# Optimization experiments

Measured on AMD Instinct MI355X. Metric: run time of the kernel, lower is better.

The kernel has to match this reference:

```python
import jax, jax.numpy as jnp
import numpy as np

B, T, D, N = 32, 2048, 512, 512


def setup_inputs() -> dict:
    key = jax.random.key(0)
    ks = jax.random.split(key, 16)
    s_in = 1.0 / np.sqrt(D)
    s_h = 1.0 / np.sqrt(N)
    inp = {
        "x": jax.random.normal(ks[0], (B, T, D), dtype=jnp.float32),
        "W_i": jax.random.normal(ks[1], (D, N), dtype=jnp.float32) * s_in,
        "U_i": jax.random.normal(ks[2], (N, N), dtype=jnp.float32) * s_h,
        "W_f": jax.random.normal(ks[3], (D, N), dtype=jnp.float32) * s_in,
        "U_f": jax.random.normal(ks[4], (N, N), dtype=jnp.float32) * s_h,
        "W_g": jax.random.normal(ks[5], (D, N), dtype=jnp.float32) * s_in,
        "U_g": jax.random.normal(ks[6], (N, N), dtype=jnp.float32) * s_h,
        "W_c": jax.random.normal(ks[7], (D, N), dtype=jnp.float32) * s_in,
        "U_c": jax.random.normal(ks[8], (N, N), dtype=jnp.float32) * s_h,
        "W_o": jax.random.normal(ks[9], (N, N), dtype=jnp.float32) * s_h,
        "b_i": jnp.zeros((N,), dtype=jnp.float32),
        "b_f": jnp.zeros((N,), dtype=jnp.float32),
        "b_g": jnp.zeros((N,), dtype=jnp.float32),
        "b_c": jnp.zeros((N,), dtype=jnp.float32),
        "b_o": jnp.zeros((N,), dtype=jnp.float32),
    }
    return inp


def _lstm_forward(x, W_i, U_i, W_f, U_f, W_g, U_g, W_c, U_c, W_o,
                  b_i, b_f, b_g, b_c, b_o):
    # Precompute input-to-gate projections for all timesteps (same math,
    # hoisted out of the recurrence): [T, B, N] each
    xt = jnp.swapaxes(x, 0, 1)  # [T, B, N? no, D] -> [T, B, D]
    xi = jnp.einsum('tbd,dn->tbn', xt, W_i) + b_i
    xf = jnp.einsum('tbd,dn->tbn', xt, W_f) + b_f
    xg = jnp.einsum('tbd,dn->tbn', xt, W_g) + b_g
    xc = jnp.einsum('tbd,dn->tbn', xt, W_c) + b_c

    h0 = jnp.zeros((x.shape[0], U_i.shape[0]), dtype=x.dtype)
    c0 = jnp.zeros_like(h0)

    def step(carry, gates_t):
        h, c = carry
        xi_t, xf_t, xg_t, xc_t = gates_t
        i = jax.nn.sigmoid(xi_t + h @ U_i)
        f = jax.nn.sigmoid(xf_t + h @ U_f)
        g = jax.nn.sigmoid(xg_t + h @ U_g)  # original applies nonlin_i to g
        c_tilda = jnp.tanh(xc_t + h @ U_c)
        c_new = f * c + i * c_tilda
        h_new = g * jnp.tanh(c_new)
        return (h_new, c_new), h_new

    _, hs = jax.lax.scan(step, (h0, c0), (xi, xf, xg, xc))  # hs: [T, B, N]
    # output_fn: relu(h @ W_o + b_o), applied per timestep
    out = jax.nn.relu(jnp.einsum('tbn,nm->tbm', hs, W_o) + b_o)
    return jnp.swapaxes(out, 0, 1)  # [B, T, N]


def reference(x, W_i, U_i, W_f, U_f, W_g, U_g, W_c, U_c, W_o,
              b_i, b_f, b_g, b_c, b_o):
    return _lstm_forward(x, W_i, U_i, W_f, U_f, W_g, U_g, W_c, U_c, W_o,
                         b_i, b_f, b_g, b_c, b_o)
```

## Files before the change

### kernel.cpp

```cpp
#include <hip/hip_runtime.h>
#include <stdint.h>

#define B_ 32
#define T_ 2048
#define D_ 512
#define N_ 512
#define NG 2048

typedef _Float16 f16;
typedef _Float16 half2v __attribute__((ext_vector_type(2)));
typedef _Float16 half8  __attribute__((ext_vector_type(8)));
typedef float    float4v __attribute__((ext_vector_type(4)));
typedef unsigned long long u64;

union U32H2 { unsigned u; half2v h; };
union U4H8  { uint4 u; half8 h; };
union H16U  { f16 h; unsigned short s; };

__global__ void prep_cast(const float* __restrict__ x, f16* __restrict__ x16) {
    long i = ((long)blockIdx.x * 256 + threadIdx.x) * 4;
    float4 v = *(const float4*)(x + i);
    union { f16 h[4]; uint2 u; } pk;
    pk.h[0] = (f16)v.x; pk.h[1] = (f16)v.y; pk.h[2] = (f16)v.z; pk.h[3] = (f16)v.w;
    *(uint2*)(x16 + i) = pk.u;
}

__global__ void prep_w(const float* __restrict__ Wi, const float* __restrict__ Ui,
                       const float* __restrict__ Wf, const float* __restrict__ Uf,
                       const float* __restrict__ Wg, const float* __restrict__ Ug,
                       const float* __restrict__ Wc, const float* __restrict__ Uc,
                       const float* __restrict__ Wo,
                       const float* __restrict__ bi, const float* __restrict__ bff,
                       const float* __restrict__ bg, const float* __restrict__ bc,
                       f16* __restrict__ wt, f16* __restrict__ ut,
                       f16* __restrict__ wot, float* __restrict__ bias)
{
    const int y = blockIdx.y;
    const int e = blockIdx.x * 256 + threadIdx.x;
    if (y < 4) {
        const float* src = (y == 0) ? Wi : (y == 1) ? Wf : (y == 2) ? Wg : Wc;
        int col = e >> 9, d = e & 511;
        wt[(long)y * 512 * 512 + e] = (f16)src[(long)d * 512 + col];
    } else if (y < 8) {
        const float* src = (y == 4) ? Ui : (y == 5) ? Uf : (y == 6) ? Ug : Uc;
        int col = e >> 9, d = e & 511;
        ut[(long)(y - 4) * 512 * 512 + e] = (f16)src[(long)d * 512 + col];
    } else if (y == 8) {
        int col = e >> 9, d = e & 511;
        wot[e] = (f16)Wo[(long)d * 512 + col];
    } else {
        if (e < 2048) {
            const float* bsrc = (e < 512) ? bi : (e < 1024) ? bff : (e < 1536) ? bg : bc;
            bias[e] = bsrc[e & 511];
        }
    }
}

__launch_bounds__(256)
__global__ void gemm_xw(const f16* __restrict__ A, const f16* __restrict__ Bt,
                        const float* __restrict__ bias, f16* __restrict__ C)
{
    __shared__ f16 sA[128 * 32];
    __shared__ f16 sB[128 * 32];
    const int tid = threadIdx.x;
    const int m0 = blockIdx.y * 128;
    const int n0 = blockIdx.x * 128;
    const int wave = tid >> 6, lane = tid & 63;
    const int wm = wave >> 1, wn = wave & 1;
    const int lrow = lane & 15, quad = lane >> 4;

    float4v acc[4][4];
#pragma unroll
    for (int i = 0; i < 4; i++)
#pragma unroll
        for (int j = 0; j < 4; j++) acc[i][j] = (float4v){0.f, 0.f, 0.f, 0.f};

    const int srow = tid >> 2;
    const int sk8 = (tid & 3) * 8;

    for (int k0 = 0; k0 < 512; k0 += 32) {
#pragma unroll
        for (int rr = 0; rr < 128; rr += 64) {
            const int row = rr + srow;
            *(uint4*)&sA[row * 32 + sk8] = *(const uint4*)&A[(long)(m0 + row) * 512 + k0 + sk8];
            *(uint4*)&sB[row * 32 + sk8] = *(const uint4*)&Bt[(long)(n0 + row) * 512 + k0 + sk8];
        }
        __syncthreads();
        half8 af[4], bf[4];
#pragma unroll
        for (int mi = 0; mi < 4; mi++)
            af[mi] = *(half8*)&sA[(wm * 64 + mi * 16 + lrow) * 32 + quad * 8];
#pragma unroll
        for (int ni = 0; ni < 4; ni++)
            bf[ni] = *(half8*)&sB[(wn * 64 + ni * 16 + lrow) * 32 + quad * 8];
#pragma unroll
        for (int mi = 0; mi < 4; mi++)
#pragma unroll
            for (int ni = 0; ni < 4; ni++)
                acc[mi][ni] = __builtin_amdgcn_mfma_f32_16x16x32_f16(af[mi], bf[ni], acc[mi][ni], 0, 0, 0);
        __syncthreads();
    }
#pragma unroll
    for (int mi = 0; mi < 4; mi++)
#pragma unroll
        for (int ni = 0; ni < 4; ni++)
#pragma unroll
            for (int r = 0; r < 4; r++) {
                int m = m0 + wm * 64 + mi * 16 + quad * 4 + r;
                int n = n0 + wn * 64 + ni * 16 + lrow;
                C[(long)m * NG + n] = (f16)(acc[mi][ni][r] + bias[n]);
            }
}

__launch_bounds__(256)
__global__ void gemm_hw(const f16* __restrict__ A, const f16* __restrict__ Bt,
                        const float* __restrict__ bias, float* __restrict__ out)
{
    __shared__ f16 sA[128 * 32];
    __shared__ f16 sB[128 * 32];
    const int tid = threadIdx.x;
    const int m0 = blockIdx.y * 128;
    const int n0 = blockIdx.x * 128;
    const int wave = tid >> 6, lane = tid & 63;
    const int wm = wave >> 1, wn = wave & 1;
    const int lrow = lane & 15, quad = lane >> 4;

    float4v acc[4][4];
#pragma unroll
    for (int i = 0; i < 4; i++)
#pragma unroll
        for (int j = 0; j < 4; j++) acc[i][j] = (float4v){0.f, 0.f, 0.f, 0.f};

    const int srow = tid >> 2;
    const int sk8 = (tid & 3) * 8;

    for (int k0 = 0; k0 < 512; k0 += 32) {
#pragma unroll
        for (int rr = 0; rr < 128; rr += 64) {
            const int row = rr + srow;
            *(uint4*)&sA[row * 32 + sk8] = *(const uint4*)&A[(long)(m0 + row) * 512 + k0 + sk8];
            *(uint4*)&sB[row * 32 + sk8] = *(const uint4*)&Bt[(long)(n0 + row) * 512 + k0 + sk8];
        }
        __syncthreads();
        half8 af[4], bf[4];
#pragma unroll
        for (int mi = 0; mi < 4; mi++)
            af[mi] = *(half8*)&sA[(wm * 64 + mi * 16 + lrow) * 32 + quad * 8];
#pragma unroll
        for (int ni = 0; ni < 4; ni++)
            bf[ni] = *(half8*)&sB[(wn * 64 + ni * 16 + lrow) * 32 + quad * 8];
#pragma unroll
        for (int mi = 0; mi < 4; mi++)
#pragma unroll
            for (int ni = 0; ni < 4; ni++)
                acc[mi][ni] = __builtin_amdgcn_mfma_f32_16x16x32_f16(af[mi], bf[ni], acc[mi][ni], 0, 0, 0);
        __syncthreads();
    }
#pragma unroll
    for (int mi = 0; mi < 4; mi++)
#pragma unroll
        for (int ni = 0; ni < 4; ni++)
#pragma unroll
            for (int r = 0; r < 4; r++) {
                int m = m0 + wm * 64 + mi * 16 + quad * 4 + r;
                int n = n0 + wn * 64 + ni * 16 + lrow;
                float v = acc[mi][ni][r] + bias[n];
                v = fmaxf(v, 0.f);
                int t = m >> 5, b = m & 31;
                out[(long)b * (T_ * (long)N_) + (long)t * N_ + n] = v;
            }
}

__launch_bounds__(256, 1)
__global__ void lstm_rec(const f16* __restrict__ Ut,
                         const f16* __restrict__ xpre,
                         u64* __restrict__ hg64,
                         unsigned* __restrict__ hs32,
                         int unused)
{
    const int tid = threadIdx.x;
    const int bb = blockIdx.x & 31;
    const int s  = blockIdx.x >> 5;
    const int w    = tid >> 6;
    const int lane = tid & 63;
    const int quad = lane >> 4;
    const int lcol = lane & 15;

    __shared__ __align__(16) unsigned hbuf32[256];

    const int ncol = s * 64 + w * 16 + lcol;
    half8 bf[4][16];
#pragma unroll
    for (int g = 0; g < 4; g++) {
        const f16* bp = Ut + ((long)(g * 512 + ncol)) * 512 + quad * 8;
#pragma unroll
        for (int ks = 0; ks < 16; ks++)
            bf[g][ks] = *(const half8*)(bp + ks * 32);
    }

    hbuf32[tid] = 0u;
    float cst = 0.f;

    const f16* xb = xpre + (long)bb * T_ * NG + quad * 512 + ncol;
    f16 xcA = xb[0];
    f16 xcB = xb[NG];
    __syncthreads();

    const int pslot = s * 32 + w * 8 + (lane & 7);

#pragma unroll 1
    for (int t2 = 0; t2 < T_; t2 += 2) {
#pragma unroll
        for (int half = 0; half < 2; half++) {
            const int t = t2 + half;
            const f16 xuse = half ? xcB : xcA;

            if (t > 0) {
                const u64* slot = hg64 + (size_t)(t & 1) * 8192 + bb * 256 + tid;
                const unsigned tag = (unsigned)t;
                u64 v;
                while ((unsigned)((v = __hip_atomic_load(slot, __ATOMIC_RELAXED,
                                                         __HIP_MEMORY_SCOPE_AGENT)) >> 32) != tag) {}
                __builtin_amdgcn_sched_barrier(0);
                {
                    const long ti = (t + 2 < T_) ? (t + 2) : (T_ - 1);
                    const f16 xn = xb[ti * NG];
                    if (half) xcB = xn; else xcA = xn;
                }
                hbuf32[tid] = (unsigned)v;
            } else {
                const f16 xn = xb[2L * NG];
                xcA = xn;
            }

            asm volatile("s_waitcnt lgkmcnt(0)" ::: "memory");
            __builtin_amdgcn_s_barrier();
            __builtin_amdgcn_sched_barrier(0);

            float4v a0 = {0.f, 0.f, 0.f, 0.f}, a1 = {0.f, 0.f, 0.f, 0.f};
            float4v a2 = {0.f, 0.f, 0.f, 0.f}, a3 = {0.f, 0.f, 0.f, 0.f};
#pragma unroll
            for (int ks = 0; ks < 16; ks++) {
                U4H8 av;
                av.u = *(const uint4*)&hbuf32[ks * 16 + quad * 4];
                a0 = __builtin_amdgcn_mfma_f32_16x16x32_f16(av.h, bf[0][ks], a0, 0, 0, 0);
                a1 = __builtin_amdgcn_mfma_f32_16x16x32_f16(av.h, bf[1][ks], a1, 0, 0, 0);
                a2 = __builtin_amdgcn_mfma_f32_16x16x32_f16(av.h, bf[2][ks], a2, 0, 0, 0);
                a3 = __builtin_amdgcn_mfma_f32_16x16x32_f16(av.h, bf[3][ks], a3, 0, 0, 0);
            }

            float p01 = (quad == 0) ? a0[0] : a1[0];
            float p23 = (quad == 2) ? a2[0] : a3[0];
            float pre = ((quad < 2) ? p01 : p23) + (float)xuse;
            float m   = (quad == 3) ? 2.f : -1.f;
            float e   = __expf(m * pre);
            float r   = __builtin_amdgcn_rcpf(1.f + e);
            float act = (quad == 3) ? 1.f - 2.f * r : r;
            float b1 = __shfl_xor(act, 16);
            float b2 = __shfl_xor(act, 32);
            float b3 = __shfl_xor(b1, 32);
            float gi = (quad == 0) ? act : (quad == 1) ? b1 : (quad == 2) ? b2 : b3;
            float gf = (quad == 1) ? act : (quad == 0) ? b1 : (quad == 3) ? b2 : b3;
            float gg = (quad == 2) ? act : (quad == 3) ? b1 : (quad == 0) ? b2 : b3;
            float ct = (quad == 3) ? act : (quad == 2) ? b1 : (quad == 1) ? b2 : b3;

            cst = gf * cst + gi * ct;
            float e2 = __expf(2.f * cst);
            float th = 1.f - 2.f * __builtin_amdgcn_rcpf(1.f + e2);
            float h  = gg * th;

            H16U cv; cv.h = (f16)h;
            unsigned hx = (unsigned)cv.s;
            unsigned lo = __shfl(hx, 2 * (lane & 7));
            unsigned hi = __shfl(hx, 2 * (lane & 7) + 1);
            if (lane < 8) {
                unsigned pk = lo | (hi << 16);
                u64 pv = ((u64)(unsigned)(t + 1) << 32) | (u64)pk;
                __hip_atomic_store(hg64 + (size_t)((t + 1) & 1) * 8192 + bb * 256 + pslot,
                                   pv, __ATOMIC_RELAXED, __HIP_MEMORY_SCOPE_AGENT);
                hs32[((long)t * B_ + bb) * 256 + pslot] = pk;
            }

            __builtin_amdgcn_sched_barrier(0);
            __builtin_amdgcn_s_barrier();
        }
    }
}

extern "C" void kernel_launch(void* const* d_in, const int* in_sizes, int n_in,
                              void* d_out, int out_size, void* d_ws, size_t ws_size,
                              hipStream_t stream)
{
    const float* x  = (const float*)d_in[0];
    const float* Wi = (const float*)d_in[1];
    const float* Ui = (const float*)d_in[2];
    const float* Wf = (const float*)d_in[3];
    const float* Uf = (const float*)d_in[4];
    const float* Wg = (const float*)d_in[5];
    const float* Ug = (const float*)d_in[6];
    const float* Wc = (const float*)d_in[7];
    const float* Uc = (const float*)d_in[8];
    const float* Wo = (const float*)d_in[9];
    const float* bi = (const float*)d_in[10];
    const float* bf = (const float*)d_in[11];
    const float* bg = (const float*)d_in[12];
    const float* bc = (const float*)d_in[13];
    const float* bo = (const float*)d_in[14];

    char* ws = (char*)d_ws;
    f16*      x16   = (f16*)(ws + 0L);
    f16*      xpre  = (f16*)(ws + 67108864L);
    f16*      hs    = (f16*)(ws + 335544320L);
    f16*      wt    = (f16*)(ws + 402653184L);
    f16*      ut    = (f16*)(ws + 404750336L);
    f16*      wot   = (f16*)(ws + 406847488L);
    float*    bias  = (float*)(ws + 407371776L);
    u64*      hg64  = (u64*)(ws + 407379968L);

    prep_cast<<<dim3(32768), dim3(256), 0, stream>>>(x, x16);
    prep_w<<<dim3(1024, 10), dim3(256), 0, stream>>>(Wi, Ui, Wf, Uf, Wg, Ug, Wc, Uc, Wo,
                                                     bi, bf, bg, bc, wt, ut, wot, bias);
    gemm_xw<<<dim3(16, 512), dim3(256), 0, stream>>>(x16, wt, bias, xpre);
    lstm_rec<<<dim3(256), dim3(256), 0, stream>>>(ut, xpre, hg64, (unsigned*)hs, 0);
    gemm_hw<<<dim3(4, 512), dim3(256), 0, stream>>>(hs, wot, bo, (float*)d_out);
}
```

Baseline: 4.040 ms.

## Batch 16 sequences per recurrent block so MFMA rows carry real batches

The recurrent kernel is reorganized so each active block handles 16 batch elements and a 64-column slice across all four gates. This fills the 16 MFMA rows with real batch rows instead of the one useful row per block before, and cuts the number of cooperating blocks from 256 to 16. Gate pre-activations go through an LDS staging buffer, with a swizzled h layout to limit bank conflicts. The trade-offs are an extra block barrier per step, a larger polled hidden-state read per thread (16 atomic loads), and a launch where three quarters of the blocks exit immediately.

```diff
diff --git a/kernel.cpp b/kernel.cpp
--- a/kernel.cpp
+++ b/kernel.cpp
@@ -16,6 +16,13 @@
 union U32H2 { unsigned u; half2v h; };
 union U4H8  { uint4 u; half8 h; };
 union H16U  { f16 h; unsigned short s; };
+
+static __device__ __forceinline__ float fast_sigmoid(float x) {
+    return __builtin_amdgcn_rcpf(1.f + __expf(-x));
+}
+static __device__ __forceinline__ float fast_tanh(float x) {
+    return 1.f - 2.f * __builtin_amdgcn_rcpf(1.f + __expf(2.f * x));
+}
 
 __global__ void prep_cast(const float* __restrict__ x, f16* __restrict__ x16) {
     long i = ((long)blockIdx.x * 256 + threadIdx.x) * 4;
@@ -178,112 +185,177 @@
                          unsigned* __restrict__ hs32,
                          int unused)
 {
-    const int tid = threadIdx.x;
-    const int bb = blockIdx.x & 31;
-    const int s  = blockIdx.x >> 5;
-    const int w    = tid >> 6;
+    if ((blockIdx.x & 7) >= 2) return;
+    const int group = blockIdx.x & 7;
+    const int slice = blockIdx.x >> 3;
+    const int n0 = slice * 64;
+
+    const int tid  = threadIdx.x;
+    const int g    = tid >> 6;
     const int lane = tid & 63;
     const int quad = lane >> 4;
     const int lcol = lane & 15;
 
-    __shared__ __align__(16) unsigned hbuf32[256];
-
-    const int ncol = s * 64 + w * 16 + lcol;
+    __shared__ __align__(16) unsigned hbuf[4096];
+    __shared__ float prelds[4224];
+
     half8 bf[4][16];
 #pragma unroll
-    for (int g = 0; g < 4; g++) {
-        const f16* bp = Ut + ((long)(g * 512 + ncol)) * 512 + quad * 8;
+    for (int nt = 0; nt < 4; nt++) {
+        const f16* bp = Ut + (long)(g * 512 + n0 + nt * 16 + lcol) * 512 + quad * 8;
 #pragma unroll
         for (int ks = 0; ks < 16; ks++)
-            bf[g][ks] = *(const half8*)(bp + ks * 32);
-    }
-
-    hbuf32[tid] = 0u;
-    float cst = 0.f;
-
-    const f16* xb = xpre + (long)bb * T_ * NG + quad * 512 + ncol;
-    f16 xcA = xb[0];
-    f16 xcB = xb[NG];
+            bf[nt][ks] = *(const half8*)(bp + ks * 32);
+    }
+
+#pragma unroll
+    for (int i = 0; i < 16; i++) hbuf[tid * 16 + i] = 0u;
+
+    const int b   = tid >> 4;
+    const int tau = tid & 15;
+    const int bglobal = group * 16 + b;
+    const int sw = (b & 7) << 2;
+
+    float cs00 = 0.f, cs01 = 0.f, cs10 = 0.f, cs11 = 0.f;
+
+    const unsigned* xq = (const unsigned*)(xpre + (long)bglobal * T_ * NG + n0);
+    unsigned xc[8], xn[8];
+#pragma unroll
+    for (int gg = 0; gg < 4; gg++)
+#pragma unroll
+        for (int j = 0; j < 2; j++)
+            xc[gg * 2 + j] = xq[gg * 256 + tau + j * 16];
+
     __syncthreads();
 
-    const int pslot = s * 32 + w * 8 + (lane & 7);
-
 #pragma unroll 1
-    for (int t2 = 0; t2 < T_; t2 += 2) {
-#pragma unroll
-        for (int half = 0; half < 2; half++) {
-            const int t = t2 + half;
-            const f16 xuse = half ? xcB : xcA;
-
-            if (t > 0) {
-                const u64* slot = hg64 + (size_t)(t & 1) * 8192 + bb * 256 + tid;
-                const unsigned tag = (unsigned)t;
-                u64 v;
-                while ((unsigned)((v = __hip_atomic_load(slot, __ATOMIC_RELAXED,
-                                                         __HIP_MEMORY_SCOPE_AGENT)) >> 32) != tag) {}
-                __builtin_amdgcn_sched_barrier(0);
-                {
-                    const long ti = (t + 2 < T_) ? (t + 2) : (T_ - 1);
-                    const f16 xn = xb[ti * NG];
-                    if (half) xcB = xn; else xcA = xn;
-                }
-                hbuf32[tid] = (unsigned)v;
+    for (int t = 0; t < T_; ++t) {
+        if (t > 0) {
+            const u64* base = hg64 + (size_t)(t & 1) * 8192 + (size_t)group * 4096 + (size_t)tid * 16;
+            const unsigned tag = (unsigned)t;
+            u64 v[16];
+#pragma unroll
+            for (int i = 0; i < 16; i++)
+                v[i] = __hip_atomic_load(base + i, __ATOMIC_RELAXED, __HIP_MEMORY_SCOPE_AGENT);
+#pragma unroll
+            for (int i = 0; i < 16; i++)
+                while ((unsigned)(v[i] >> 32) != tag)
+                    v[i] = __hip_atomic_load(base + i, __ATOMIC_RELAXED, __HIP_MEMORY_SCOPE_AGENT);
+            __builtin_amdgcn_sched_barrier(0);
+
+            {
+                const long tn = (t + 1 < T_) ? (t + 1) : t;
+#pragma unroll
+                for (int gg = 0; gg < 4; gg++)
+#pragma unroll
+                    for (int j = 0; j < 2; j++)
+                        xn[gg * 2 + j] = xq[tn * 1024 + gg * 256 + tau + j * 16];
+            }
+
+            const int p0 = tau * 16;
+#pragma unroll
+            for (int c = 0; c < 4; c++) {
+                uint4 d;
+                d.x = (unsigned)v[c * 4 + 0];
+                d.y = (unsigned)v[c * 4 + 1];
+                d.z = (unsigned)v[c * 4 + 2];
+                d.w = (unsigned)v[c * 4 + 3];
+                *(uint4*)&hbuf[b * 256 + ((p0 + c * 4) ^ sw)] = d;
+            }
+        } else {
+#pragma unroll
+            for (int gg = 0; gg < 4; gg++)
+#pragma unroll
+                for (int j = 0; j < 2; j++)
+                    xn[gg * 2 + j] = xq[1024 + gg * 256 + tau + j * 16];
+        }
+
+        asm volatile("s_waitcnt lgkmcnt(0)" ::: "memory");
+        __builtin_amdgcn_s_barrier();
+        __builtin_amdgcn_sched_barrier(0);
+
+        uint4 av[16];
+        {
+            const int swb = (lcol & 7) << 2;
+#pragma unroll
+            for (int ks = 0; ks < 16; ks++)
+                av[ks] = *(const uint4*)&hbuf[lcol * 256 + (((ks * 16 + quad * 4)) ^ swb)];
+        }
+        float4v ae[4], ao[4];
+#pragma unroll
+        for (int nt = 0; nt < 4; nt++) {
+            ae[nt] = (float4v){0.f, 0.f, 0.f, 0.f};
+            ao[nt] = (float4v){0.f, 0.f, 0.f, 0.f};
+        }
+#pragma unroll
+        for (int ks = 0; ks < 16; ks++) {
+            U4H8 a; a.u = av[ks];
+            if (ks & 1) {
+#pragma unroll
+                for (int nt = 0; nt < 4; nt++)
+                    ao[nt] = __builtin_amdgcn_mfma_f32_16x16x32_f16(a.h, bf[nt][ks], ao[nt], 0, 0, 0);
             } else {
-                const f16 xn = xb[2L * NG];
-                xcA = xn;
-            }
-
-            asm volatile("s_waitcnt lgkmcnt(0)" ::: "memory");
-            __builtin_amdgcn_s_barrier();
-            __builtin_amdgcn_sched_barrier(0);
-
-            float4v a0 = {0.f, 0.f, 0.f, 0.f}, a1 = {0.f, 0.f, 0.f, 0.f};
-            float4v a2 = {0.f, 0.f, 0.f, 0.f}, a3 = {0.f, 0.f, 0.f, 0.f};
-#pragma unroll
-            for (int ks = 0; ks < 16; ks++) {
-                U4H8 av;
-                av.u = *(const uint4*)&hbuf32[ks * 16 + quad * 4];
-                a0 = __builtin_amdgcn_mfma_f32_16x16x32_f16(av.h, bf[0][ks], a0, 0, 0, 0);
-                a1 = __builtin_amdgcn_mfma_f32_16x16x32_f16(av.h, bf[1][ks], a1, 0, 0, 0);
-                a2 = __builtin_amdgcn_mfma_f32_16x16x32_f16(av.h, bf[2][ks], a2, 0, 0, 0);
-                a3 = __builtin_amdgcn_mfma_f32_16x16x32_f16(av.h, bf[3][ks], a3, 0, 0, 0);
-            }
-
-            float p01 = (quad == 0) ? a0[0] : a1[0];
-            float p23 = (quad == 2) ? a2[0] : a3[0];
-            float pre = ((quad < 2) ? p01 : p23) + (float)xuse;
-            float m   = (quad == 3) ? 2.f : -1.f;
-            float e   = __expf(m * pre);
-            float r   = __builtin_amdgcn_rcpf(1.f + e);
-            float act = (quad == 3) ? 1.f - 2.f * r : r;
-            float b1 = __shfl_xor(act, 16);
-            float b2 = __shfl_xor(act, 32);
-            float b3 = __shfl_xor(b1, 32);
-            float gi = (quad == 0) ? act : (quad == 1) ? b1 : (quad == 2) ? b2 : b3;
-            float gf = (quad == 1) ? act : (quad == 0) ? b1 : (quad == 3) ? b2 : b3;
-            float gg = (quad == 2) ? act : (quad == 3) ? b1 : (quad == 0) ? b2 : b3;
-            float ct = (quad == 3) ? act : (quad == 2) ? b1 : (quad == 1) ? b2 : b3;
-
-            cst = gf * cst + gi * ct;
-            float e2 = __expf(2.f * cst);
-            float th = 1.f - 2.f * __builtin_amdgcn_rcpf(1.f + e2);
-            float h  = gg * th;
-
-            H16U cv; cv.h = (f16)h;
-            unsigned hx = (unsigned)cv.s;
-            unsigned lo = __shfl(hx, 2 * (lane & 7));
-            unsigned hi = __shfl(hx, 2 * (lane & 7) + 1);
-            if (lane < 8) {
-                unsigned pk = lo | (hi << 16);
-                u64 pv = ((u64)(unsigned)(t + 1) << 32) | (u64)pk;
-                __hip_atomic_store(hg64 + (size_t)((t + 1) & 1) * 8192 + bb * 256 + pslot,
-                                   pv, __ATOMIC_RELAXED, __HIP_MEMORY_SCOPE_AGENT);
-                hs32[((long)t * B_ + bb) * 256 + pslot] = pk;
-            }
-
-            __builtin_amdgcn_sched_barrier(0);
-            __builtin_amdgcn_s_barrier();
-        }
+#pragma unroll
+                for (int nt = 0; nt < 4; nt++)
+                    ae[nt] = __builtin_amdgcn_mfma_f32_16x16x32_f16(a.h, bf[nt][ks], ae[nt], 0, 0, 0);
+            }
+        }
+
+#pragma unroll
+        for (int nt = 0; nt < 4; nt++) {
+            float4v s;
+#pragma unroll
+            for (int r = 0; r < 4; r++) s[r] = ae[nt][r] + ao[nt][r];
+#pragma unroll
+            for (int r = 0; r < 4; r++)
+                prelds[g * 1056 + (quad * 4 + r) * 66 + nt * 16 + lcol] = s[r];
+        }
+
+        asm volatile("s_waitcnt lgkmcnt(0)" ::: "memory");
+        __builtin_amdgcn_s_barrier();
+        __builtin_amdgcn_sched_barrier(0);
+
+#pragma unroll
+        for (int j = 0; j < 2; j++) {
+            const int np = tau + j * 16;
+            const float* pb = prelds + b * 66 + 2 * np;
+            float2 Pi = *(const float2*)(pb);
+            float2 Pf = *(const float2*)(pb + 1056);
+            float2 Pg = *(const float2*)(pb + 2112);
+            float2 Pc = *(const float2*)(pb + 3168);
+            U32H2 xi, xf, xg, xcc;
+            xi.u = xc[0 * 2 + j]; xf.u = xc[1 * 2 + j];
+            xg.u = xc[2 * 2 + j]; xcc.u = xc[3 * 2 + j];
+
+            float gi0 = fast_sigmoid(Pi.x + (float)xi.h[0]);
+            float gi1 = fast_sigmoid(Pi.y + (float)xi.h[1]);
+            float gf0 = fast_sigmoid(Pf.x + (float)xf.h[0]);
+            float gf1 = fast_sigmoid(Pf.y + (float)xf.h[1]);
+            float gg0 = fast_sigmoid(Pg.x + (float)xg.h[0]);
+            float gg1 = fast_sigmoid(Pg.y + (float)xg.h[1]);
+            float ct0 = fast_tanh(Pc.x + (float)xcc.h[0]);
+            float ct1 = fast_tanh(Pc.y + (float)xcc.h[1]);
+
+            float c0 = (j == 0) ? cs00 : cs10;
+            float c1 = (j == 0) ? cs01 : cs11;
+            c0 = gf0 * c0 + gi0 * ct0;
+            c1 = gf1 * c1 + gi1 * ct1;
+            if (j == 0) { cs00 = c0; cs01 = c1; } else { cs10 = c0; cs11 = c1; }
+
+            float h0 = gg0 * fast_tanh(c0);
+            float h1 = gg1 * fast_tanh(c1);
+
+            H16U u0, u1; u0.h = (f16)h0; u1.h = (f16)h1;
+            unsigned pk = (unsigned)u0.s | ((unsigned)u1.s << 16);
+            u64 pv = ((u64)(unsigned)(t + 1) << 32) | (u64)pk;
+            const int pair = slice * 32 + np;
+            __hip_atomic_store(hg64 + (size_t)((t + 1) & 1) * 8192 + (size_t)bglobal * 256 + pair,
+                               pv, __ATOMIC_RELAXED, __HIP_MEMORY_SCOPE_AGENT);
+            hs32[((long)t * B_ + bglobal) * 256 + pair] = pk;
+        }
+
+#pragma unroll
+        for (int k = 0; k < 8; k++) xc[k] = xn[k];
     }
 }
 
@@ -321,6 +393,6 @@
     prep_w<<<dim3(1024, 10), dim3(256), 0, stream>>>(Wi, Ui, Wf, Uf, Wg, Ug, Wc, Uc, Wo,
                                                      bi, bf, bg, bc, wt, ut, wot, bias);
     gemm_xw<<<dim3(16, 512), dim3(256), 0, stream>>>(x16, wt, bias, xpre);
-    lstm_rec<<<dim3(256), dim3(256), 0, stream>>>(ut, xpre, hg64, (unsigned*)hs, 0);
+    lstm_rec<<<dim3(64), dim3(256), 0, stream>>>(ut, xpre, hg64, (unsigned*)hs, 0);
     gemm_hw<<<dim3(4, 512), dim3(256), 0, stream>>>(hs, wot, bo, (float*)d_out);
 }
```

Result: slower. 14.02 ms (+247.1%).
